# Kernel tuning notes

Hardware: AMD Instinct MI355X
Metric: run time of the kernel (lower is better)

## Reference

```python
import itertools
import jax, jax.numpy as jnp
import numpy as np

LATENT_DIM = 8
N = 2 * LATENT_DIM  # width of z_combined = concat([z, dz])
BATCH = 131072

# Static combinatorial index sets, matching the nested-loop order
# (i <= j [<= k]) of the torch implementation exactly.
_PAIRS = np.array(list(itertools.combinations_with_replacement(range(N), 2)), dtype=np.int32)   # [136, 2]
_TRIPLES = np.array(list(itertools.combinations_with_replacement(range(N), 3)), dtype=np.int32)  # [816, 3]


def setup_inputs() -> dict:
    key = jax.random.key(0)
    k1, k2 = jax.random.split(key)
    z = jax.random.normal(k1, (BATCH, LATENT_DIM), dtype=jnp.float32)
    dz = jax.random.normal(k2, (BATCH, LATENT_DIM), dtype=jnp.float32)
    return {"z": z, "dz": dz}


def reference(z, dz):
    # z, dz: [B, latent_dim] -> Theta: [B, 985]
    zc = jnp.concatenate([z, dz], axis=1)  # [B, N]
    B = zc.shape[0]
    ones = jnp.ones((B, 1), dtype=zc.dtype)
    # degree-2 terms: zc[:, i] * zc[:, j] for i <= j, all at once via gather
    deg2 = zc[:, _PAIRS[:, 0]] * zc[:, _PAIRS[:, 1]]  # [B, 136]
    # degree-3 terms: zc[:, i] * zc[:, j] * zc[:, k] for i <= j <= k
    deg3 = zc[:, _TRIPLES[:, 0]] * zc[:, _TRIPLES[:, 1]] * zc[:, _TRIPLES[:, 2]]  # [B, 816]
    sine = jnp.sin(zc)  # [B, N]
    return jnp.concatenate([ones, zc, deg2, deg3, sine], axis=1)  # [B, 985]
```

## Files before the change

### kernel.cpp

```cpp
#include <hip/hip_runtime.h>
#include <cstddef>

#define NCOLS 985
#define RPW   16
#define GSTR  176

__global__ __launch_bounds__(256) void sindy_kernel(const float* __restrict__ z,
                                                    const float* __restrict__ dz,
                                                    float* __restrict__ out, int batch) {
  __shared__ unsigned short mtab[1024];
  __shared__ unsigned short ptab[136];
  __shared__ float G[4][GSTR];

  const int tid = threadIdx.x;

  for (int e = tid; e < 1024; e += 256) {
    int a, b;
    if (e < 153)       { a = (e == 0) ? 0 : e; b = 0; }
    else if (e < 969)  {
      int t = e - 153, i = 0;
      for (;;) { int c = (16 - i) * (17 - i) / 2; if (t < c) break; t -= c; ++i; }
      int j = i; while (t >= 16 - j) { t -= 16 - j; ++j; }
      int k = j + t;
      int p = i * 16 - i * (i - 1) / 2 + (j - i);
      a = 17 + p; b = 1 + k;
    }
    else if (e < 985)  { a = 153 + (e - 969); b = 0; }
    else               { a = 169; b = 169; }
    mtab[e] = (unsigned short)(a | (b << 8));
  }
  for (int e = tid; e < 136; e += 256) {
    int p = e, i = 0; while (p >= 16 - i) { p -= 16 - i; ++i; }
    ptab[e] = (unsigned short)(i | ((i + p) << 4));
  }
  __syncthreads();

  const int w = tid >> 6, l = tid & 63;

  unsigned short mt[16];
  #pragma unroll
  for (int wd = 0; wd < 16; ++wd) mt[wd] = mtab[wd * 64 + l];
  const unsigned pe0 = ptab[l];
  const unsigned pe1 = ptab[64 + l];
  const unsigned pe2 = ptab[(128 + l < 136) ? (128 + l) : 135];

  float* Gw = G[w];
  const int row0 = (blockIdx.x * 4 + w) * RPW;
  if (row0 >= batch) return;

  for (int rr = 0; rr < RPW; ++rr) {
    const int row = row0 + rr;
    if (row >= batch) break;

    float gval = 0.f;
    if (l == 0)       gval = 1.0f;
    else if (l < 9)   gval = z [(size_t)row * 8 + (l - 1)];
    else if (l < 17)  gval = dz[(size_t)row * 8 + (l - 9)];
    const int gaddr = (l < 17) ? l : (152 + l);
    if (l < 24) Gw[gaddr] = gval;

    const float sv = __shfl(gval, l + 1);
    if (l < 16) Gw[153 + l] = __sinf(sv);
    __builtin_amdgcn_sched_barrier(0);

    {
      float a0 = Gw[1 + (pe0 & 15)], b0 = Gw[1 + (pe0 >> 4)];
      Gw[17 + l] = a0 * b0;
      float a1 = Gw[1 + (pe1 & 15)], b1 = Gw[1 + (pe1 >> 4)];
      Gw[17 + 64 + l] = a1 * b1;
      if (l < 8) {
        float a2 = Gw[1 + (pe2 & 15)], b2 = Gw[1 + (pe2 >> 4)];
        Gw[17 + 128 + l] = a2 * b2;
      }
    }
    __builtin_amdgcn_sched_barrier(0);

    float* orow = out + (size_t)row * NCOLS;
    #pragma unroll
    for (int wd = 0; wd < 16; ++wd) {
      const unsigned e = mt[wd];
      const float v = Gw[e & 255] * Gw[e >> 8];
      if (wd < 15)                 orow[wd * 64 + l] = v;
      else if (l < NCOLS - 960)    orow[960 + l] = v;
    }
    __builtin_amdgcn_sched_barrier(0);
  }
}

extern "C" void kernel_launch(void* const* d_in, const int* in_sizes, int n_in,
                              void* d_out, int out_size, void* d_ws, size_t ws_size,
                              hipStream_t stream) {
  const float* z  = (const float*)d_in[0];
  const float* dz = (const float*)d_in[1];
  float* out = (float*)d_out;
  const int batch = in_sizes[0] / 8;

  const int blocks = (batch + 4 * RPW - 1) / (4 * RPW);
  sindy_kernel<<<blocks, 256, 0, stream>>>(z, dz, out, batch);
}
```

Measured before the change: 128.9 us.

## Stage 4-row slabs in LDS and store with float4 via persistent grid

```diff
diff --git a/kernel.cpp b/kernel.cpp
--- a/kernel.cpp
+++ b/kernel.cpp
@@ -2,15 +2,19 @@
 #include <cstddef>
 
 #define NCOLS 985
-#define RPW   16
+#define SROWS 4
+#define SLABF (SROWS * NCOLS)
+#define NQ4   (SLABF / 4)
 #define GSTR  176
 
 __global__ __launch_bounds__(256) void sindy_kernel(const float* __restrict__ z,
                                                     const float* __restrict__ dz,
-                                                    float* __restrict__ out, int batch) {
+                                                    float* __restrict__ out, int batch,
+                                                    int nsup, int nwaves) {
   __shared__ unsigned short mtab[1024];
   __shared__ unsigned short ptab[136];
   __shared__ float G[4][GSTR];
+  __shared__ alignas(16) float slab[4][SLABF];
 
   const int tid = threadIdx.x;
 
@@ -45,43 +49,62 @@
   const unsigned pe2 = ptab[(128 + l < 136) ? (128 + l) : 135];
 
   float* Gw = G[w];
-  const int row0 = (blockIdx.x * 4 + w) * RPW;
-  if (row0 >= batch) return;
+  float* sw = slab[w];
+  const int gwave = blockIdx.x * 4 + w;
 
-  for (int rr = 0; rr < RPW; ++rr) {
-    const int row = row0 + rr;
-    if (row >= batch) break;
+  for (int st = gwave; st < nsup; st += nwaves) {
+    const int row0 = st * SROWS;
 
-    float gval = 0.f;
-    if (l == 0)       gval = 1.0f;
-    else if (l < 9)   gval = z [(size_t)row * 8 + (l - 1)];
-    else if (l < 17)  gval = dz[(size_t)row * 8 + (l - 9)];
-    const int gaddr = (l < 17) ? l : (152 + l);
-    if (l < 24) Gw[gaddr] = gval;
+    #pragma unroll
+    for (int rr = 0; rr < SROWS; ++rr) {
+      const int row = row0 + rr;
+      if (row < batch) {
+        float gval = 0.f;
+        if (l == 0)       gval = 1.0f;
+        else if (l < 9)   gval = z [(size_t)row * 8 + (l - 1)];
+        else if (l < 17)  gval = dz[(size_t)row * 8 + (l - 9)];
+        const int gaddr = (l < 17) ? l : (152 + l);
+        if (l < 24) Gw[gaddr] = gval;
 
-    const float sv = __shfl(gval, l + 1);
-    if (l < 16) Gw[153 + l] = __sinf(sv);
-    __builtin_amdgcn_sched_barrier(0);
+        const float sv = __shfl(gval, l + 1);
+        if (l < 16) Gw[153 + l] = __sinf(sv);
+        __builtin_amdgcn_sched_barrier(0);
 
-    {
-      float a0 = Gw[1 + (pe0 & 15)], b0 = Gw[1 + (pe0 >> 4)];
-      Gw[17 + l] = a0 * b0;
-      float a1 = Gw[1 + (pe1 & 15)], b1 = Gw[1 + (pe1 >> 4)];
-      Gw[17 + 64 + l] = a1 * b1;
-      if (l < 8) {
-        float a2 = Gw[1 + (pe2 & 15)], b2 = Gw[1 + (pe2 >> 4)];
-        Gw[17 + 128 + l] = a2 * b2;
+        {
+          float a0 = Gw[1 + (pe0 & 15)], b0 = Gw[1 + (pe0 >> 4)];
+          Gw[17 + l] = a0 * b0;
+          float a1 = Gw[1 + (pe1 & 15)], b1 = Gw[1 + (pe1 >> 4)];
+          Gw[17 + 64 + l] = a1 * b1;
+          if (l < 8) {
+            float a2 = Gw[1 + (pe2 & 15)], b2 = Gw[1 + (pe2 >> 4)];
+            Gw[17 + 128 + l] = a2 * b2;
+          }
+        }
+        __builtin_amdgcn_sched_barrier(0);
+
+        float* rb = sw + rr * NCOLS;
+        #pragma unroll
+        for (int wd = 0; wd < 16; ++wd) {
+          const unsigned e = mt[wd];
+          const float v = Gw[e & 255] * Gw[e >> 8];
+          if (wd < 15)              rb[wd * 64 + l] = v;
+          else if (l < NCOLS - 960) rb[960 + l] = v;
+        }
+        __builtin_amdgcn_sched_barrier(0);
       }
     }
-    __builtin_amdgcn_sched_barrier(0);
 
-    float* orow = out + (size_t)row * NCOLS;
-    #pragma unroll
-    for (int wd = 0; wd < 16; ++wd) {
-      const unsigned e = mt[wd];
-      const float v = Gw[e & 255] * Gw[e >> 8];
-      if (wd < 15)                 orow[wd * 64 + l] = v;
-      else if (l < NCOLS - 960)    orow[960 + l] = v;
+    if (row0 + SROWS <= batch) {
+      float4* __restrict__ dst = (float4*)(out + (size_t)row0 * NCOLS);
+      const float4* srcq = (const float4*)sw;
+      #pragma unroll 4
+      for (int u = l; u < NQ4; u += 64) {
+        dst[u] = srcq[u];
+      }
+    } else {
+      const int nel = (batch - row0) * NCOLS;
+      float* __restrict__ dst = out + (size_t)row0 * NCOLS;
+      for (int u = l; u < nel; u += 64) dst[u] = sw[u];
     }
     __builtin_amdgcn_sched_barrier(0);
   }
@@ -95,6 +118,8 @@
   float* out = (float*)d_out;
   const int batch = in_sizes[0] / 8;
 
-  const int blocks = (batch + 4 * RPW - 1) / (4 * RPW);
-  sindy_kernel<<<blocks, 256, 0, stream>>>(z, dz, out, batch);
+  const int nsup   = (batch + SROWS - 1) / SROWS;
+  const int blocks = 512;
+  const int nwaves = blocks * 4;
+  sindy_kernel<<<blocks, 256, 0, stream>>>(z, dz, out, batch, nsup, nwaves);
 }
```

Result: slower. 133.7 us (+3.7%).

## Process 4-row groups per wave with float4 stores and grid-stride loop

Applied to the files above, without the earlier changes.

```diff
diff --git a/kernel.cpp b/kernel.cpp
--- a/kernel.cpp
+++ b/kernel.cpp
@@ -1,33 +1,38 @@
 #include <hip/hip_runtime.h>
 #include <cstddef>
 
-#define NCOLS 985
-#define RPW   16
-#define GSTR  176
+#define NCOLS  985
+#define GROWS  4
+#define GFLT   (GROWS * NCOLS)
+#define NU     (GFLT / 4)
+#define GSTR   176
 
 __global__ __launch_bounds__(256) void sindy_kernel(const float* __restrict__ z,
                                                     const float* __restrict__ dz,
-                                                    float* __restrict__ out, int batch) {
-  __shared__ unsigned short mtab[1024];
+                                                    float* __restrict__ out, int batch,
+                                                    int ngroups, int nwaves) {
+  __shared__ alignas(16) unsigned int utab[GFLT];
   __shared__ unsigned short ptab[136];
-  __shared__ float G[4][GSTR];
+  __shared__ float G4[4][GROWS * GSTR];
 
   const int tid = threadIdx.x;
 
-  for (int e = tid; e < 1024; e += 256) {
+  for (int fe = tid; fe < GFLT; fe += 256) {
+    const int r   = fe / NCOLS;
+    const int col = fe - r * NCOLS;
     int a, b;
-    if (e < 153)       { a = (e == 0) ? 0 : e; b = 0; }
-    else if (e < 969)  {
-      int t = e - 153, i = 0;
+    if (col < 153)      { a = (col == 0) ? 0 : col; b = 0; }
+    else if (col < 969) {
+      int t = col - 153, i = 0;
       for (;;) { int c = (16 - i) * (17 - i) / 2; if (t < c) break; t -= c; ++i; }
       int j = i; while (t >= 16 - j) { t -= 16 - j; ++j; }
       int k = j + t;
       int p = i * 16 - i * (i - 1) / 2 + (j - i);
       a = 17 + p; b = 1 + k;
     }
-    else if (e < 985)  { a = 153 + (e - 969); b = 0; }
-    else               { a = 169; b = 169; }
-    mtab[e] = (unsigned short)(a | (b << 8));
+    else                { a = 153 + (col - 969); b = 0; }
+    const unsigned base = (unsigned)(r * GSTR);
+    utab[fe] = (base + (unsigned)a) | ((base + (unsigned)b) << 16);
   }
   for (int e = tid; e < 136; e += 256) {
     int p = e, i = 0; while (p >= 16 - i) { p -= 16 - i; ++i; }
@@ -37,53 +42,96 @@
 
   const int w = tid >> 6, l = tid & 63;
 
-  unsigned short mt[16];
-  #pragma unroll
-  for (int wd = 0; wd < 16; ++wd) mt[wd] = mtab[wd * 64 + l];
   const unsigned pe0 = ptab[l];
   const unsigned pe1 = ptab[64 + l];
   const unsigned pe2 = ptab[(128 + l < 136) ? (128 + l) : 135];
 
-  float* Gw = G[w];
-  const int row0 = (blockIdx.x * 4 + w) * RPW;
-  if (row0 >= batch) return;
+  float* Gw = G4[w];
+  const int gwave = blockIdx.x * 4 + w;
 
-  for (int rr = 0; rr < RPW; ++rr) {
-    const int row = row0 + rr;
-    if (row >= batch) break;
+  for (int grp = gwave; grp < ngroups; grp += nwaves) {
+    const int row0 = grp * GROWS;
 
-    float gval = 0.f;
-    if (l == 0)       gval = 1.0f;
-    else if (l < 9)   gval = z [(size_t)row * 8 + (l - 1)];
-    else if (l < 17)  gval = dz[(size_t)row * 8 + (l - 9)];
-    const int gaddr = (l < 17) ? l : (152 + l);
-    if (l < 24) Gw[gaddr] = gval;
+    #pragma unroll
+    for (int rr = 0; rr < GROWS; ++rr) {
+      const int row = row0 + rr;
+      float gval = 0.f;
+      if (l == 0)       gval = 1.0f;
+      else if (l < 9)   gval = z [(size_t)row * 8 + (l - 1)];
+      else if (l < 17)  gval = dz[(size_t)row * 8 + (l - 9)];
+      float* Gr = Gw + rr * GSTR;
+      const int gaddr = (l < 17) ? l : (152 + l);
+      if (l < 24) Gr[gaddr] = gval;
 
-    const float sv = __shfl(gval, l + 1);
-    if (l < 16) Gw[153 + l] = __sinf(sv);
-    __builtin_amdgcn_sched_barrier(0);
+      const float sv = __shfl(gval, l + 1);
+      if (l < 16) Gr[153 + l] = __sinf(sv);
+      __builtin_amdgcn_sched_barrier(0);
 
-    {
-      float a0 = Gw[1 + (pe0 & 15)], b0 = Gw[1 + (pe0 >> 4)];
-      Gw[17 + l] = a0 * b0;
-      float a1 = Gw[1 + (pe1 & 15)], b1 = Gw[1 + (pe1 >> 4)];
-      Gw[17 + 64 + l] = a1 * b1;
-      if (l < 8) {
-        float a2 = Gw[1 + (pe2 & 15)], b2 = Gw[1 + (pe2 >> 4)];
-        Gw[17 + 128 + l] = a2 * b2;
+      {
+        float a0 = Gr[1 + (pe0 & 15)], b0 = Gr[1 + (pe0 >> 4)];
+        Gr[17 + l] = a0 * b0;
+        float a1 = Gr[1 + (pe1 & 15)], b1 = Gr[1 + (pe1 >> 4)];
+        Gr[17 + 64 + l] = a1 * b1;
+        if (l < 8) {
+          float a2 = Gr[1 + (pe2 & 15)], b2 = Gr[1 + (pe2 >> 4)];
+          Gr[17 + 128 + l] = a2 * b2;
+        }
+      }
+      __builtin_amdgcn_sched_barrier(0);
+    }
+
+    float4* __restrict__ dst = (float4*)(out + (size_t)row0 * NCOLS);
+    const uint4* ut = (const uint4*)utab;
+    #pragma unroll
+    for (int it = 0; it < 16; ++it) {
+      const int u = it * 64 + l;
+      if (it < 15 || l < NU - 960) {
+        const uint4 e = ut[u];
+        float4 v;
+        v.x = Gw[e.x & 0xffffu] * Gw[e.x >> 16];
+        v.y = Gw[e.y & 0xffffu] * Gw[e.y >> 16];
+        v.z = Gw[e.z & 0xffffu] * Gw[e.z >> 16];
+        v.w = Gw[e.w & 0xffffu] * Gw[e.w >> 16];
+        dst[u] = v;
       }
     }
     __builtin_amdgcn_sched_barrier(0);
+  }
 
-    float* orow = out + (size_t)row * NCOLS;
-    #pragma unroll
-    for (int wd = 0; wd < 16; ++wd) {
-      const unsigned e = mt[wd];
-      const float v = Gw[e & 255] * Gw[e >> 8];
-      if (wd < 15)                 orow[wd * 64 + l] = v;
-      else if (l < NCOLS - 960)    orow[960 + l] = v;
+  const int rem0 = ngroups * GROWS;
+  if (rem0 < batch && gwave == 0) {
+    for (int row = rem0; row < batch; ++row) {
+      float gval = 0.f;
+      if (l == 0)       gval = 1.0f;
+      else if (l < 9)   gval = z [(size_t)row * 8 + (l - 1)];
+      else if (l < 17)  gval = dz[(size_t)row * 8 + (l - 9)];
+      float* Gr = Gw;
+      const int gaddr = (l < 17) ? l : (152 + l);
+      if (l < 24) Gr[gaddr] = gval;
+      const float sv = __shfl(gval, l + 1);
+      if (l < 16) Gr[153 + l] = __sinf(sv);
+      __builtin_amdgcn_sched_barrier(0);
+      {
+        float a0 = Gr[1 + (pe0 & 15)], b0 = Gr[1 + (pe0 >> 4)];
+        Gr[17 + l] = a0 * b0;
+        float a1 = Gr[1 + (pe1 & 15)], b1 = Gr[1 + (pe1 >> 4)];
+        Gr[17 + 64 + l] = a1 * b1;
+        if (l < 8) {
+          float a2 = Gr[1 + (pe2 & 15)], b2 = Gr[1 + (pe2 >> 4)];
+          Gr[17 + 128 + l] = a2 * b2;
+        }
+      }
+      __builtin_amdgcn_sched_barrier(0);
+      float* orow = out + (size_t)row * NCOLS;
+      for (int wd = 0; wd < 16; ++wd) {
+        const int col = wd * 64 + l;
+        if (col < NCOLS) {
+          const unsigned e = utab[col];
+          orow[col] = Gw[e & 0xffffu] * Gw[e >> 16];
+        }
+      }
+      __builtin_amdgcn_sched_barrier(0);
     }
-    __builtin_amdgcn_sched_barrier(0);
   }
 }
 
@@ -95,6 +143,8 @@
   float* out = (float*)d_out;
   const int batch = in_sizes[0] / 8;
 
-  const int blocks = (batch + 4 * RPW - 1) / (4 * RPW);
-  sindy_kernel<<<blocks, 256, 0, stream>>>(z, dz, out, batch);
+  const int blocks  = 2048;
+  const int nwaves  = blocks * 4;
+  const int ngroups = batch / GROWS;
+  sindy_kernel<<<blocks, 256, 0, stream>>>(z, dz, out, batch, ngroups, nwaves);
 }
```

New measurement: 127.8 us. About the same (-0.9%).
